# Kernel tuning notes

Measured on AMD Instinct MI355X. Metric: run time of the kernel, lower is better.

## Reference

```python
import jax, jax.numpy as jnp
import numpy as np

EMBED = 512
HEADS = 8                      # num_heads
HD = EMBED // HEADS // 2       # diff-attn head dim = 32
EXP = 4
DEPTH = 1
LAMBDA_INIT = 0.8 - 0.6 * float(np.exp(-0.3 * (DEPTH - 1)))  # 0.2
EPS = 1e-5


def layernorm(x, w, b):
    mu = jnp.mean(x, axis=-1, keepdims=True)
    var = jnp.mean(jnp.square(x - mu), axis=-1, keepdims=True)
    return (x - mu) * jax.lax.rsqrt(var + EPS) * w + b


def rmsnorm(x, w):
    ms = jnp.mean(jnp.square(x), axis=-1, keepdims=True)
    return x * jax.lax.rsqrt(ms + EPS) * w


def setup_inputs() -> dict:
    key = jax.random.key(0)
    ks = jax.random.split(key, 12)
    B, N, D = 8, 1024, EMBED
    s = 0.02
    inp = {
        "x": jax.random.normal(ks[0], (B, N, D), jnp.float32),
        # diff-attention params
        "Wq": jax.random.normal(ks[1], (D, D), jnp.float32) * s,
        "Wk": jax.random.normal(ks[2], (D, D), jnp.float32) * s,
        "Wv": jax.random.normal(ks[3], (D, D), jnp.float32) * s,
        "Wo": jax.random.normal(ks[4], (D, D), jnp.float32) * s,
        "lq1": jax.random.normal(ks[5], (HD,), jnp.float32) * 0.1,
        "lk1": jax.random.normal(ks[6], (HD,), jnp.float32) * 0.1,
        "lq2": jax.random.normal(ks[7], (HD,), jnp.float32) * 0.1,
        "lk2": jax.random.normal(ks[8], (HD,), jnp.float32) * 0.1,
        "subln_w": jnp.ones((2 * HD,), jnp.float32),
        # block norms
        "n1_w": jnp.ones((D,), jnp.float32), "n1_b": jnp.zeros((D,), jnp.float32),
        "n2_w": jnp.ones((D,), jnp.float32), "n2_b": jnp.zeros((D,), jnp.float32),
        # MLP: LN(D) -> Linear(D,4D) -> GELU -> LN(4D) -> Linear(4D,D)
        "mln1_w": jnp.ones((D,), jnp.float32), "mln1_b": jnp.zeros((D,), jnp.float32),
        "mW1": jax.random.normal(ks[9], (EXP * D, D), jnp.float32) * s,
        "mb1": jnp.zeros((EXP * D,), jnp.float32),
        "mln2_w": jnp.ones((EXP * D,), jnp.float32), "mln2_b": jnp.zeros((EXP * D,), jnp.float32),
        "mW2": jax.random.normal(ks[10], (D, EXP * D), jnp.float32) * s,
        "mb2": jnp.zeros((D,), jnp.float32),
    }
    return inp


def diff_attn(x, Wq, Wk, Wv, Wo, lq1, lk1, lq2, lk2, subln_w):
    B, N, D = x.shape
    q = (x @ Wq.T).reshape(B, N, 2 * HEADS, HD).transpose(0, 2, 1, 3)   # [B,2H,N,hd]
    k = (x @ Wk.T).reshape(B, N, 2 * HEADS, HD).transpose(0, 2, 1, 3)   # [B,2H,N,hd]
    v = (x @ Wv.T).reshape(B, N, HEADS, 2 * HD).transpose(0, 2, 1, 3)   # [B,H,N,2hd]
    q = q * (HD ** -0.5)
    scores = jnp.einsum("bhnd,bhmd->bhnm", q, k)                        # [B,2H,N,N]
    attn = jax.nn.softmax(scores, axis=-1)
    attn = attn.reshape(B, HEADS, 2, N, N)
    lam1 = jnp.exp(jnp.sum(lq1 * lk1))
    lam2 = jnp.exp(jnp.sum(lq2 * lk2))
    lam = lam1 - lam2 + LAMBDA_INIT
    attn = attn[:, :, 0] - lam * attn[:, :, 1]                          # [B,H,N,N]
    out = jnp.einsum("bhnm,bhmd->bhnd", attn, v)                        # [B,H,N,2hd]
    out = rmsnorm(out, subln_w) * (1.0 - LAMBDA_INIT)
    out = out.transpose(0, 2, 1, 3).reshape(B, N, D)
    return out @ Wo.T


def reference(x, Wq, Wk, Wv, Wo, lq1, lk1, lq2, lk2, subln_w,
              n1_w, n1_b, n2_w, n2_b,
              mln1_w, mln1_b, mW1, mb1, mln2_w, mln2_b, mW2, mb2):
    x_res = x
    xn = layernorm(x, n1_w, n1_b)
    a = diff_attn(xn, Wq, Wk, Wv, Wo, lq1, lk1, lq2, lk2, subln_w)
    h = layernorm(a, n2_w, n2_b) + x_res
    # MLP
    z = layernorm(h, mln1_w, mln1_b)
    z = jax.nn.gelu(z @ mW1.T + mb1, approximate=False)
    z = layernorm(z, mln2_w, mln2_b)
    z = z @ mW2.T + mb2
    return z + h
```

## Files before the change

### kernel.cpp

```cpp
#include <hip/hip_runtime.h>
#include <cstdint>
#include <cstddef>

typedef unsigned short u16;
typedef unsigned int   u32;
typedef __attribute__((ext_vector_type(8))) short short8;
typedef __attribute__((ext_vector_type(4))) float floatx4;

__device__ __forceinline__ float asf(u32 u){ union{u32 u; float f;} v; v.u=u; return v.f; }
__device__ __forceinline__ u32 asu(float f){ union{float f; u32 u;} v; v.f=f; return v.u; }
__device__ __forceinline__ u16 f2bf(float f){ u32 u = asu(f); u32 r = u + 0x7FFFu + ((u>>16)&1u); return (u16)(r>>16); }
__device__ __forceinline__ u16 f2bf_fast(float f){ return (u16)((asu(f) + 0x8000u)>>16); }
__device__ __forceinline__ u32 pack2(float a, float b){ return (u32)f2bf(a) | (((u32)f2bf(b))<<16); }
__device__ __forceinline__ void bf8f(uint4 d, float* o){
  o[0]=asf(d.x<<16); o[1]=asf(d.x&0xFFFF0000u);
  o[2]=asf(d.y<<16); o[3]=asf(d.y&0xFFFF0000u);
  o[4]=asf(d.z<<16); o[5]=asf(d.z&0xFFFF0000u);
  o[6]=asf(d.w<<16); o[7]=asf(d.w&0xFFFF0000u);
}

__global__ __launch_bounds__(256) void cvt_all(
    const float* __restrict__ Wq, const float* __restrict__ Wk,
    const float* __restrict__ Wv, const float* __restrict__ Wo,
    const float* __restrict__ W1, const float* __restrict__ W2,
    u16* __restrict__ Wqkv, u16* __restrict__ Wob,
    u16* __restrict__ W1b, u16* __restrict__ W2b)
{
  const int blk = blockIdx.x;
  const float* src; u16* dst; int off;
  if      (blk < 128)  { src = Wq; dst = Wqkv;          off = blk; }
  else if (blk < 256)  { src = Wk; dst = Wqkv + 262144; off = blk - 128; }
  else if (blk < 384)  { src = Wv; dst = Wqkv + 524288; off = blk - 256; }
  else if (blk < 512)  { src = Wo; dst = Wob;           off = blk - 384; }
  else if (blk < 1024) { src = W1; dst = W1b;           off = blk - 512; }
  else                 { src = W2; dst = W2b;           off = blk - 1024; }
  const int i = (off*256 + threadIdx.x)*8;
  const float4 a = *(const float4*)(src + i);
  const float4 b = *(const float4*)(src + i + 4);
  uint4 st;
  st.x = pack2(a.x, a.y); st.y = pack2(a.z, a.w);
  st.z = pack2(b.x, b.y); st.w = pack2(b.z, b.w);
  *(uint4*)(dst + i) = st;
}

enum { EPI_NONE=0, EPI_BIAS_GELU=1, EPI_BIAS_RES=2 };

template<int BM, int EPI, typename OutT>
__global__ __launch_bounds__(256) void gemm_bt(
    const u16* __restrict__ A, const u16* __restrict__ B,
    const float* __restrict__ bias, const float* __restrict__ res,
    OutT* __restrict__ C, int M, int N, int K)
{
  __shared__ u16 As[2][BM*32];
  __shared__ u16 Bs[2][128*32];
  const int tid  = threadIdx.x;
  const int wave = tid >> 6;
  const int lane = tid & 63;
  const int bm = blockIdx.y, bn = blockIdx.x;

  const int srow = wave*16 + (lane>>2);
  const int scol = (lane&3)*8;
  const u16* Ag = A + (size_t)bm*BM*K;
  const u16* Bg = B + (size_t)bn*128*K;

  constexpr int WM = BM/2;
  constexpr int MI = WM/16;
  const int wm = (wave>>1)*WM;
  const int wn = (wave&1)*64;
  const int fr = lane & 15;
  const int fk = (lane>>4)*8;

  floatx4 acc[MI][4] = {};

  #define G_STAGE(buf, kk)                                                        \
    do {                                                                          \
      if constexpr (BM == 128) {                                                  \
        _Pragma("unroll")                                                         \
        for (int tt = 0; tt < 2; ++tt)                                            \
          __builtin_amdgcn_global_load_lds(                                       \
              (__attribute__((address_space(1))) void*)(Ag + (tt*64 + srow)*K + (kk) + scol), \
              (__attribute__((address_space(3))) void*)(&As[buf][(tt*64 + wave*16)*32]),      \
              16, 0, 0);                                                          \
      } else {                                                                    \
        __builtin_amdgcn_global_load_lds(                                         \
            (__attribute__((address_space(1))) void*)(Ag + srow*K + (kk) + scol), \
            (__attribute__((address_space(3))) void*)(&As[buf][wave*16*32]),      \
            16, 0, 0);                                                            \
      }                                                                           \
      _Pragma("unroll")                                                           \
      for (int tt = 0; tt < 2; ++tt)                                              \
        __builtin_amdgcn_global_load_lds(                                         \
            (__attribute__((address_space(1))) void*)(Bg + (tt*64 + srow)*K + (kk) + scol), \
            (__attribute__((address_space(3))) void*)(&Bs[buf][(tt*64 + wave*16)*32]),      \
            16, 0, 0);                                                            \
    } while (0)

  G_STAGE(0, 0);
  __syncthreads();

  const int nsteps = K >> 5;
  for (int s = 0; s < nsteps; ++s) {
    const int cur = s & 1;
    if (s + 1 < nsteps) G_STAGE(cur^1, (s+1)*32);

    short8 af[MI], bfr[4];
    #pragma unroll
    for (int i=0;i<MI;i++) af[i] = *(const short8*)(&As[cur][(wm + i*16 + fr)*32 + fk]);
    #pragma unroll
    for (int j=0;j<4;j++) bfr[j] = *(const short8*)(&Bs[cur][(wn + j*16 + fr)*32 + fk]);
    #pragma unroll
    for (int i=0;i<MI;i++)
      #pragma unroll
      for (int j=0;j<4;j++)
        acc[i][j] = __builtin_amdgcn_mfma_f32_16x16x32_bf16(af[i], bfr[j], acc[i][j], 0, 0, 0);

    if (s + 1 < nsteps) __syncthreads();
  }
  #undef G_STAGE

  const int col0 = bn*128 + wn + fr;
  float bv[4] = {0.f,0.f,0.f,0.f};
  if constexpr (EPI != EPI_NONE) {
    #pragma unroll
    for (int j=0;j<4;j++) bv[j] = bias[col0 + j*16];
  }
  const int rq = (lane>>4)*4;
  #pragma unroll
  for (int i=0;i<MI;i++){
    #pragma unroll
    for (int rr=0;rr<4;rr++){
      const int m = bm*BM + wm + i*16 + rq + rr;
      const size_t rowoff = (size_t)m*N;
      #pragma unroll
      for (int j=0;j<4;j++){
        float vv = acc[i][j][rr];
        const int n = col0 + j*16;
        if constexpr (EPI == EPI_BIAS_GELU){
          vv += bv[j];
          vv = 0.5f*vv*(1.f + erff(vv*0.70710678118654752f));
        } else if constexpr (EPI == EPI_BIAS_RES){
          vv += bv[j] + res[rowoff + n];
        }
        if constexpr (sizeof(OutT) == 2) C[rowoff + n] = f2bf(vv);
        else                             C[rowoff + n] = vv;
      }
    }
  }
}

__global__ __launch_bounds__(256) void ln512_kernel(
    const float* __restrict__ x, const float* __restrict__ w, const float* __restrict__ b,
    u16* __restrict__ out)
{
  const int row  = blockIdx.x*4 + (threadIdx.x>>6);
  const int lane = threadIdx.x & 63;
  const size_t base = (size_t)row*512 + lane*8;
  float v[8];
  { const float4 a = *(const float4*)(x + base);
    const float4 c = *(const float4*)(x + base + 4);
    v[0]=a.x; v[1]=a.y; v[2]=a.z; v[3]=a.w; v[4]=c.x; v[5]=c.y; v[6]=c.z; v[7]=c.w; }
  float s=0.f, sq=0.f;
  #pragma unroll
  for (int i=0;i<8;i++){ s += v[i]; sq += v[i]*v[i]; }
  for (int off=32; off>0; off>>=1){ s += __shfl_xor(s, off, 64); sq += __shfl_xor(sq, off, 64); }
  const float mu = s*(1.f/512.f);
  const float rs = rsqrtf(sq*(1.f/512.f) - mu*mu + 1e-5f);
  float o[8];
  #pragma unroll
  for (int i=0;i<8;i++)
    o[i] = (v[i]-mu)*rs*w[lane*8+i] + b[lane*8+i];
  uint4 st; st.x=pack2(o[0],o[1]); st.y=pack2(o[2],o[3]); st.z=pack2(o[4],o[5]); st.w=pack2(o[6],o[7]);
  *(uint4*)(out + base) = st;
}

__global__ __launch_bounds__(256) void lnres_kernel(
    const u16* __restrict__ ao, const float* __restrict__ x,
    const float* __restrict__ w2, const float* __restrict__ b2,
    const float* __restrict__ w3, const float* __restrict__ b3,
    float* __restrict__ h, u16* __restrict__ z)
{
  const int row  = blockIdx.x*4 + (threadIdx.x>>6);
  const int lane = threadIdx.x & 63;
  const size_t base = (size_t)row*512 + lane*8;
  float a[8], xr[8];
  bf8f(*(const uint4*)(ao + base), a);
  { const float4 p = *(const float4*)(x + base);
    const float4 q = *(const float4*)(x + base + 4);
    xr[0]=p.x; xr[1]=p.y; xr[2]=p.z; xr[3]=p.w; xr[4]=q.x; xr[5]=q.y; xr[6]=q.z; xr[7]=q.w; }
  float s=0.f, sq=0.f;
  #pragma unroll
  for (int i=0;i<8;i++){ s += a[i]; sq += a[i]*a[i]; }
  for (int off=32; off>0; off>>=1){ s += __shfl_xor(s, off, 64); sq += __shfl_xor(sq, off, 64); }
  float mu = s*(1.f/512.f);
  float rs = rsqrtf(sq*(1.f/512.f) - mu*mu + 1e-5f);
  float hv[8];
  #pragma unroll
  for (int i=0;i<8;i++)
    hv[i] = (a[i]-mu)*rs*w2[lane*8+i] + b2[lane*8+i] + xr[i];
  { float4 p; p.x=hv[0]; p.y=hv[1]; p.z=hv[2]; p.w=hv[3];
    float4 q; q.x=hv[4]; q.y=hv[5]; q.z=hv[6]; q.w=hv[7];
    *(float4*)(h + base) = p; *(float4*)(h + base + 4) = q; }
  s=0.f; sq=0.f;
  #pragma unroll
  for (int i=0;i<8;i++){ s += hv[i]; sq += hv[i]*hv[i]; }
  for (int off=32; off>0; off>>=1){ s += __shfl_xor(s, off, 64); sq += __shfl_xor(sq, off, 64); }
  mu = s*(1.f/512.f);
  rs = rsqrtf(sq*(1.f/512.f) - mu*mu + 1e-5f);
  float zv[8];
  #pragma unroll
  for (int i=0;i<8;i++)
    zv[i] = (hv[i]-mu)*rs*w3[lane*8+i] + b3[lane*8+i];
  uint4 st; st.x=pack2(zv[0],zv[1]); st.y=pack2(zv[2],zv[3]); st.z=pack2(zv[4],zv[5]); st.w=pack2(zv[6],zv[7]);
  *(uint4*)(z + base) = st;
}

__global__ __launch_bounds__(256) void ln2048_kernel(
    const u16* x, const float* __restrict__ w, const float* __restrict__ b,
    u16* out)
{
  const int row  = blockIdx.x*4 + (threadIdx.x>>6);
  const int lane = threadIdx.x & 63;
  const u16* xp = x + (size_t)row*2048;
  float v[32];
  #pragma unroll
  for (int g=0; g<4; ++g) bf8f(*(const uint4*)(xp + g*512 + lane*8), v + g*8);
  float s=0.f, sq=0.f;
  #pragma unroll
  for (int i=0;i<32;i++){ s += v[i]; sq += v[i]*v[i]; }
  for (int off=32; off>0; off>>=1){ s += __shfl_xor(s, off, 64); sq += __shfl_xor(sq, off, 64); }
  const float mu = s*(1.f/2048.f);
  const float rs = rsqrtf(sq*(1.f/2048.f) - mu*mu + 1e-5f);
  u16* op = out + (size_t)row*2048;
  #pragma unroll
  for (int g=0; g<4; ++g){
    float o[8];
    #pragma unroll
    for (int i=0;i<8;i++){
      const int idx = g*512 + lane*8 + i;
      o[i] = (v[g*8+i]-mu)*rs*w[idx] + b[idx];
    }
    uint4 st; st.x=pack2(o[0],o[1]); st.y=pack2(o[2],o[3]); st.z=pack2(o[4],o[5]); st.w=pack2(o[6],o[7]);
    *(uint4*)(op + g*512 + lane*8) = st;
  }
}

__global__ __launch_bounds__(256) void transpose_v(
    const u16* __restrict__ QKV, u16* __restrict__ Vt)
{
  __shared__ __align__(16) u16 T[64][72];
  const int bid = blockIdx.x;
  const int bh  = bid >> 4;
  const int kt  = bid & 15;
  const int b   = bh >> 3;
  const int h   = bh & 7;
  const int tid = threadIdx.x;

  const int key = tid >> 2;
  const int dc  = (tid & 3) * 16;
  const u16* src = QKV + ((size_t)(b*1024 + kt*64 + key))*1536 + 1024 + h*64 + dc;
  const uint4 a0 = *(const uint4*)(src);
  const uint4 a1 = *(const uint4*)(src + 8);
  *(uint4*)(&T[key][dc])     = a0;
  *(uint4*)(&T[key][dc + 8]) = a1;
  __syncthreads();

  const int d  = tid >> 2;
  const int kc = (tid & 3) * 16;
  union { uint4 q[2]; u16 us[16]; } ow;
  #pragma unroll
  for (int i=0;i<16;i++) ow.us[i] = T[kc + i][d];
  u16* dst = Vt + ((size_t)(bh*64 + d))*1024 + kt*64 + kc;
  *(uint4*)(dst)     = ow.q[0];
  *(uint4*)(dst + 8) = ow.q[1];
}

#define ATT_SCALE 0.17677669529663687f

__global__ __launch_bounds__(256) void attn_mfma(
    const u16* __restrict__ QKV, const u16* __restrict__ Vt,
    const float* __restrict__ lq1, const float* __restrict__ lk1,
    const float* __restrict__ lq2, const float* __restrict__ lk2,
    const float* __restrict__ subw, u16* __restrict__ out)
{
  __shared__ __align__(16) u16 Ks1[2][64*32];
  __shared__ __align__(16) u16 Ks2[2][64*32];
  __shared__ __align__(16) u16 Vs [2][64*64];
  __shared__ __align__(16) u16 Ps [2][4][16*32];

  const int tid  = threadIdx.x;
  const int wave = tid >> 6;
  const int lane = tid & 63;
  const int quad = lane >> 4;
  const int l15  = lane & 15;

  const int bid = blockIdx.x;
  const int bh  = bid >> 4;
  const int qt  = bid & 15;
  const int b   = bh >> 3;
  const int h   = bh & 7;

  float t1 = 0.f, t2 = 0.f;
  for (int i=0;i<32;i++){ t1 += lq1[i]*lk1[i]; t2 += lq2[i]*lk2[i]; }
  const float lam = __expf(t1) - __expf(t2) + 0.2f;

  const int qrowg = b*1024 + qt*64 + wave*16 + l15;
  const short8 aq1 = *(const short8*)(QKV + (size_t)qrowg*1536 + 2*h*32 + quad*8);
  const short8 aq2 = *(const short8*)(QKV + (size_t)qrowg*1536 + 2*h*32 + 32 + quad*8);

  floatx4 O1[4] = {}, O2[4] = {};
  float l1acc[4] = {0.f,0.f,0.f,0.f};
  float l2acc[4] = {0.f,0.f,0.f,0.f};
  const floatx4 zf4 = {0.f,0.f,0.f,0.f};

  const int kvbase = b*1024;
  u16* pw1 = &Ps[0][wave][0];
  u16* pw2 = &Ps[1][wave][0];

  const int kchunk = ((lane&3) ^ ((lane>>3)&3)) * 8;
  const u16* KbaseS = QKV + (size_t)(kvbase + wave*16 + (lane>>2))*1536 + 512 + 2*h*32 + kchunk;
  const int vchunk = ((lane&7) ^ (lane>>3)) * 8;
  const u16* VbaseS = Vt + ((size_t)bh*64 + wave*16 + (lane>>3))*1024 + vchunk;

  #define STAGE_TILE(buf, tt)                                                     \
    do {                                                                          \
      const u16* kp = KbaseS + (size_t)(tt)*64*1536;                              \
      __builtin_amdgcn_global_load_lds(                                           \
          (__attribute__((address_space(1))) void*)(kp),                          \
          (__attribute__((address_space(3))) void*)(&Ks1[buf][wave*16*32]), 16, 0, 0); \
      __builtin_amdgcn_global_load_lds(                                           \
          (__attribute__((address_space(1))) void*)(kp + 32),                     \
          (__attribute__((address_space(3))) void*)(&Ks2[buf][wave*16*32]), 16, 0, 0); \
      const u16* vp = VbaseS + (tt)*64;                                           \
      __builtin_amdgcn_global_load_lds(                                           \
          (__attribute__((address_space(1))) void*)(vp),                          \
          (__attribute__((address_space(3))) void*)(&Vs[buf][wave*16*64]), 16, 0, 0); \
      __builtin_amdgcn_global_load_lds(                                           \
          (__attribute__((address_space(1))) void*)(vp + (size_t)8*1024),         \
          (__attribute__((address_space(3))) void*)(&Vs[buf][(wave*16+8)*64]), 16, 0, 0); \
    } while (0)

  STAGE_TILE(0, 0);
  __syncthreads();

  const int kslotR = (quad ^ ((l15>>1)&3)) * 8;
  const int pslotR = ((quad + (l15>>2)) & 3) * 8;

  for (int t = 0; t < 16; ++t) {
    const int cur = t & 1;

    if (t < 15) STAGE_TILE(cur^1, t+1);

    #pragma unroll
    for (int kh = 0; kh < 2; ++kh) {
      #pragma unroll
      for (int ktl = 0; ktl < 2; ++ktl) {
        const int kt = kh*2 + ktl;
        const short8 bk1 = *(const short8*)(&Ks1[cur][(kt*16 + l15)*32 + kslotR]);
        const short8 bk2 = *(const short8*)(&Ks2[cur][(kt*16 + l15)*32 + kslotR]);
        const floatx4 s1 = __builtin_amdgcn_mfma_f32_16x16x32_bf16(aq1, bk1, zf4, 0, 0, 0);
        const floatx4 s2 = __builtin_amdgcn_mfma_f32_16x16x32_bf16(aq2, bk2, zf4, 0, 0, 0);
        const int wslot = ((ktl*2 + (l15>>3) + quad) & 3)*8;
        u16* d1 = pw1 + wslot + (l15&7);
        u16* d2 = pw2 + wslot + (l15&7);
        #pragma unroll
        for (int rr = 0; rr < 4; ++rr) {
          const float p1 = __expf(s1[rr]*ATT_SCALE);
          const float p2 = __expf(s2[rr]*ATT_SCALE);
          d1[(quad*4+rr)*32] = f2bf_fast(p1);
          d2[(quad*4+rr)*32] = f2bf_fast(p2);
          l1acc[rr] += p1;
          l2acc[rr] += p2;
        }
      }
      const short8 ap1 = *(const short8*)(pw1 + l15*32 + pslotR);
      const short8 ap2 = *(const short8*)(pw2 + l15*32 + pslotR);
      const int vslotR = ((kh*4 + quad) ^ (l15&7)) * 8;
      #pragma unroll
      for (int nt = 0; nt < 4; ++nt) {
        const short8 bv = *(const short8*)(&Vs[cur][(nt*16 + l15)*64 + vslotR]);
        O1[nt] = __builtin_amdgcn_mfma_f32_16x16x32_bf16(ap1, bv, O1[nt], 0, 0, 0);
        O2[nt] = __builtin_amdgcn_mfma_f32_16x16x32_bf16(ap2, bv, O2[nt], 0, 0, 0);
      }
    }

    if (t < 15) __syncthreads();
  }
  #undef STAGE_TILE

  #pragma unroll
  for (int rr=0; rr<4; ++rr){
    float v1 = l1acc[rr], v2 = l2acc[rr];
    v1 += __shfl_xor(v1, 1, 64); v2 += __shfl_xor(v2, 1, 64);
    v1 += __shfl_xor(v1, 2, 64); v2 += __shfl_xor(v2, 2, 64);
    v1 += __shfl_xor(v1, 4, 64); v2 += __shfl_xor(v2, 4, 64);
    v1 += __shfl_xor(v1, 8, 64); v2 += __shfl_xor(v2, 8, 64);
    l1acc[rr] = v1; l2acc[rr] = v2;
  }

  float sw[4];
  #pragma unroll
  for (int nt=0; nt<4; ++nt) sw[nt] = subw[nt*16 + l15];

  #pragma unroll
  for (int rr=0; rr<4; ++rr){
    const int row = quad*4 + rr;
    const float il1 = 1.f / l1acc[rr];
    const float cl2 = lam / l2acc[rr];
    float o[4]; float ss = 0.f;
    #pragma unroll
    for (int nt=0; nt<4; ++nt){
      o[nt] = O1[nt][rr]*il1 - O2[nt][rr]*cl2;
      ss += o[nt]*o[nt];
    }
    ss += __shfl_xor(ss, 1, 64);
    ss += __shfl_xor(ss, 2, 64);
    ss += __shfl_xor(ss, 4, 64);
    ss += __shfl_xor(ss, 8, 64);
    const float rs = rsqrtf(ss*(1.f/64.f) + 1e-5f) * 0.8f;
    const int orow = b*1024 + qt*64 + wave*16 + row;
    u16* op = out + (size_t)orow*512 + h*64 + l15;
    #pragma unroll
    for (int nt=0; nt<4; ++nt)
      op[nt*16] = f2bf(o[nt]*rs*sw[nt]);
  }
}

extern "C" void kernel_launch(void* const* d_in, const int* in_sizes, int n_in,
                              void* d_out, int out_size, void* d_ws, size_t ws_size,
                              hipStream_t stream)
{
  (void)in_sizes; (void)n_in; (void)out_size; (void)ws_size;
  const float* x    = (const float*)d_in[0];
  const float* Wq   = (const float*)d_in[1];
  const float* Wk   = (const float*)d_in[2];
  const float* Wv   = (const float*)d_in[3];
  const float* Wo   = (const float*)d_in[4];
  const float* lq1  = (const float*)d_in[5];
  const float* lk1  = (const float*)d_in[6];
  const float* lq2  = (const float*)d_in[7];
  const float* lk2  = (const float*)d_in[8];
  const float* subw = (const float*)d_in[9];
  const float* n1w  = (const float*)d_in[10];
  const float* n1b  = (const float*)d_in[11];
  const float* n2w  = (const float*)d_in[12];
  const float* n2b  = (const float*)d_in[13];
  const float* m1w  = (const float*)d_in[14];
  const float* m1b  = (const float*)d_in[15];
  const float* mW1  = (const float*)d_in[16];
  const float* mb1  = (const float*)d_in[17];
  const float* m2w  = (const float*)d_in[18];
  const float* m2b  = (const float*)d_in[19];
  const float* mW2  = (const float*)d_in[20];
  const float* mb2  = (const float*)d_in[21];
  float* out = (float*)d_out;

  char* ws = (char*)d_ws;
  const size_t MB = (size_t)1 << 20;
  u16*  xn  = (u16*)(ws + 0*MB);
  u16*  qkv = (u16*)(ws + 8*MB);
  u16*  a   = (u16*)(ws + 0*MB);
  u16*  ao  = (u16*)(ws + 8*MB);
  u16*  z1  = (u16*)(ws + 16*MB);
  float* h  = (float*)(ws + 32*MB);
  u16*  vt  = (u16*)(ws + 32*MB);
  u16*  t   = (u16*)(ws + 48*MB);
  u16* Wqkvb= (u16*)(ws + 80*MB);
  u16* Wob  = (u16*)(ws + 81*MB + 512*1024);
  u16* W1b  = (u16*)(ws + 82*MB);
  u16* W2b  = (u16*)(ws + 84*MB);

  const int M = 8192;

  cvt_all<<<1536, 256, 0, stream>>>(Wq, Wk, Wv, Wo, mW1, mW2, Wqkvb, Wob, W1b, W2b);

  ln512_kernel<<<2048, 256, 0, stream>>>(x, n1w, n1b, xn);

  gemm_bt<64,EPI_NONE,u16><<<dim3(12,128), 256, 0, stream>>>(xn, Wqkvb, nullptr, nullptr, qkv, M, 1536, 512);

  transpose_v<<<1024, 256, 0, stream>>>(qkv, vt);

  attn_mfma<<<1024, 256, 0, stream>>>(qkv, vt, lq1, lk1, lq2, lk2, subw, a);

  gemm_bt<64,EPI_NONE,u16><<<dim3(4,128), 256, 0, stream>>>(a, Wob, nullptr, nullptr, ao, M, 512, 512);

  lnres_kernel<<<2048, 256, 0, stream>>>(ao, x, n2w, n2b, m1w, m1b, h, z1);

  gemm_bt<64,EPI_BIAS_GELU,u16><<<dim3(16,128), 256, 0, stream>>>(z1, W1b, mb1, nullptr, t, M, 2048, 512);

  ln2048_kernel<<<2048, 256, 0, stream>>>(t, m2w, m2b, t);

  gemm_bt<64,EPI_BIAS_RES,float><<<dim3(4,128), 256, 0, stream>>>(t, W2b, mb2, h, out, M, 512, 2048);
}
```

Baseline: 318.4 us.

## Deepen GEMM K-tile to 64 with XOR-swizzled LDS layout and remap attention blocks

The GEMM now stages 64-wide K slices instead of 32, which halves the number of barrier-synchronised steps and doubles the MFMA work done per sync. Each 16-byte chunk is placed in LDS at a column XOR-swizzled by its row, to avoid bank conflicts on the fragment reads. Shared memory per block doubles, which may reduce occupancy. The attention kernel's block-id mapping is also permuted, so neighbouring blocks handle different batch/head pairs and may spread load across XCDs or caches differently.

After: 305.2 us. -4.1%, faster.

```diff
diff --git a/kernel.cpp b/kernel.cpp
--- a/kernel.cpp
+++ b/kernel.cpp
@@ -51,15 +51,15 @@
     const float* __restrict__ bias, const float* __restrict__ res,
     OutT* __restrict__ C, int M, int N, int K)
 {
-  __shared__ u16 As[2][BM*32];
-  __shared__ u16 Bs[2][128*32];
+  __shared__ u16 As[2][BM*64];
+  __shared__ u16 Bs[2][128*64];
   const int tid  = threadIdx.x;
   const int wave = tid >> 6;
   const int lane = tid & 63;
   const int bm = blockIdx.y, bn = blockIdx.x;
 
-  const int srow = wave*16 + (lane>>2);
-  const int scol = (lane&3)*8;
+  const int srow8  = lane >> 3;
+  const int schunk = ((lane&7) ^ (lane>>3)) * 8;
   const u16* Ag = A + (size_t)bm*BM*K;
   const u16* Bg = B + (size_t)bn*128*K;
 
@@ -68,51 +68,55 @@
   const int wm = (wave>>1)*WM;
   const int wn = (wave&1)*64;
   const int fr = lane & 15;
-  const int fk = (lane>>4)*8;
+  const int quad = lane >> 4;
 
   floatx4 acc[MI][4] = {};
 
-  #define G_STAGE(buf, kk)                                                        \
+  #define G_STAGE(buf, koff)                                                      \
     do {                                                                          \
-      if constexpr (BM == 128) {                                                  \
-        _Pragma("unroll")                                                         \
-        for (int tt = 0; tt < 2; ++tt)                                            \
-          __builtin_amdgcn_global_load_lds(                                       \
-              (__attribute__((address_space(1))) void*)(Ag + (tt*64 + srow)*K + (kk) + scol), \
-              (__attribute__((address_space(3))) void*)(&As[buf][(tt*64 + wave*16)*32]),      \
-              16, 0, 0);                                                          \
-      } else {                                                                    \
+      _Pragma("unroll")                                                           \
+      for (int ii = 0; ii < BM/32; ++ii)                                          \
         __builtin_amdgcn_global_load_lds(                                         \
-            (__attribute__((address_space(1))) void*)(Ag + srow*K + (kk) + scol), \
-            (__attribute__((address_space(3))) void*)(&As[buf][wave*16*32]),      \
+            (__attribute__((address_space(1))) void*)(Ag + (size_t)(wave*(BM/4) + ii*8 + srow8)*K + (koff) + schunk), \
+            (__attribute__((address_space(3))) void*)(&As[buf][(wave*(BM/4) + ii*8)*64]), \
             16, 0, 0);                                                            \
-      }                                                                           \
       _Pragma("unroll")                                                           \
-      for (int tt = 0; tt < 2; ++tt)                                              \
+      for (int ii = 0; ii < 4; ++ii)                                              \
         __builtin_amdgcn_global_load_lds(                                         \
-            (__attribute__((address_space(1))) void*)(Bg + (tt*64 + srow)*K + (kk) + scol), \
-            (__attribute__((address_space(3))) void*)(&Bs[buf][(tt*64 + wave*16)*32]),      \
+            (__attribute__((address_space(1))) void*)(Bg + (size_t)(wave*32 + ii*8 + srow8)*K + (koff) + schunk), \
+            (__attribute__((address_space(3))) void*)(&Bs[buf][(wave*32 + ii*8)*64]), \
             16, 0, 0);                                                            \
     } while (0)
 
   G_STAGE(0, 0);
   __syncthreads();
 
-  const int nsteps = K >> 5;
+  const int nsteps = K >> 6;
   for (int s = 0; s < nsteps; ++s) {
     const int cur = s & 1;
-    if (s + 1 < nsteps) G_STAGE(cur^1, (s+1)*32);
-
-    short8 af[MI], bfr[4];
-    #pragma unroll
-    for (int i=0;i<MI;i++) af[i] = *(const short8*)(&As[cur][(wm + i*16 + fr)*32 + fk]);
-    #pragma unroll
-    for (int j=0;j<4;j++) bfr[j] = *(const short8*)(&Bs[cur][(wn + j*16 + fr)*32 + fk]);
-    #pragma unroll
-    for (int i=0;i<MI;i++)
-      #pragma unroll
-      for (int j=0;j<4;j++)
-        acc[i][j] = __builtin_amdgcn_mfma_f32_16x16x32_bf16(af[i], bfr[j], acc[i][j], 0, 0, 0);
+    if (s + 1 < nsteps) G_STAGE(cur^1, (s+1)*64);
+
+    short8 af[2][MI], bfr[2][4];
+    #pragma unroll
+    for (int kk=0; kk<2; ++kk){
+      #pragma unroll
+      for (int i=0;i<MI;i++){
+        const int row = wm + i*16 + fr;
+        af[kk][i] = *(const short8*)(&As[cur][row*64 + (((kk*4+quad) ^ (fr&7))*8)]);
+      }
+      #pragma unroll
+      for (int j=0;j<4;j++){
+        const int row = wn + j*16 + fr;
+        bfr[kk][j] = *(const short8*)(&Bs[cur][row*64 + (((kk*4+quad) ^ (fr&7))*8)]);
+      }
+    }
+    #pragma unroll
+    for (int kk=0; kk<2; ++kk)
+      #pragma unroll
+      for (int i=0;i<MI;i++)
+        #pragma unroll
+        for (int j=0;j<4;j++)
+          acc[i][j] = __builtin_amdgcn_mfma_f32_16x16x32_bf16(af[kk][i], bfr[kk][j], acc[i][j], 0, 0, 0);
 
     if (s + 1 < nsteps) __syncthreads();
   }
@@ -294,8 +298,8 @@
   const int l15  = lane & 15;
 
   const int bid = blockIdx.x;
-  const int bh  = bid >> 4;
-  const int qt  = bid & 15;
+  const int bh  = (bid & 7)*8 + ((bid >> 3) >> 4);
+  const int qt  = (bid >> 3) & 15;
   const int b   = bh >> 3;
   const int h   = bh & 7;
 
```

## Swizzle GEMM LDS layout, fold softmax scale into Q, remap attention blocks

Applied to the files above, without the earlier changes.

The GEMM tile staging now writes rows in an XOR-swizzled chunk order and reads them back with the matching swizzle, meant to remove LDS bank conflicts on the MFMA fragment loads. The QKV projection gains an epilogue that scales Q columns by scale*log2(e), so the attention kernel can use exp2f without a per-element multiply. The attention block index is remapped to interleave batch/head across consecutive blocks, which changes how work spreads over compute units and caches. The extra rounding from scaling Q before bf16 conversion slightly changes numerics.

New measurement: 323.4 us. Within noise of the previous version (+1.6%).

```diff
diff --git a/kernel.cpp b/kernel.cpp
--- a/kernel.cpp
+++ b/kernel.cpp
@@ -18,6 +18,8 @@
   o[4]=asf(d.z<<16); o[5]=asf(d.z&0xFFFF0000u);
   o[6]=asf(d.w<<16); o[7]=asf(d.w&0xFFFF0000u);
 }
+
+#define SC2 0.25503485966f
 
 __global__ __launch_bounds__(256) void cvt_all(
     const float* __restrict__ Wq, const float* __restrict__ Wk,
@@ -43,7 +45,7 @@
   *(uint4*)(dst + i) = st;
 }
 
-enum { EPI_NONE=0, EPI_BIAS_GELU=1, EPI_BIAS_RES=2 };
+enum { EPI_NONE=0, EPI_BIAS_GELU=1, EPI_BIAS_RES=2, EPI_QSCALE=3 };
 
 template<int BM, int EPI, typename OutT>
 __global__ __launch_bounds__(256) void gemm_bt(
@@ -58,8 +60,8 @@
   const int lane = tid & 63;
   const int bm = blockIdx.y, bn = blockIdx.x;
 
-  const int srow = wave*16 + (lane>>2);
-  const int scol = (lane&3)*8;
+  const int srow   = lane >> 2;
+  const int schunk = ((lane&3) ^ ((lane>>3)&3)) * 8;
   const u16* Ag = A + (size_t)bm*BM*K;
   const u16* Bg = B + (size_t)bn*128*K;
 
@@ -68,36 +70,30 @@
   const int wm = (wave>>1)*WM;
   const int wn = (wave&1)*64;
   const int fr = lane & 15;
-  const int fk = (lane>>4)*8;
+  const int quad = lane >> 4;
 
   floatx4 acc[MI][4] = {};
 
   #define G_STAGE(buf, kk)                                                        \
     do {                                                                          \
-      if constexpr (BM == 128) {                                                  \
-        _Pragma("unroll")                                                         \
-        for (int tt = 0; tt < 2; ++tt)                                            \
-          __builtin_amdgcn_global_load_lds(                                       \
-              (__attribute__((address_space(1))) void*)(Ag + (tt*64 + srow)*K + (kk) + scol), \
-              (__attribute__((address_space(3))) void*)(&As[buf][(tt*64 + wave*16)*32]),      \
-              16, 0, 0);                                                          \
-      } else {                                                                    \
+      _Pragma("unroll")                                                           \
+      for (int ii = 0; ii < BM/64; ++ii)                                          \
         __builtin_amdgcn_global_load_lds(                                         \
-            (__attribute__((address_space(1))) void*)(Ag + srow*K + (kk) + scol), \
-            (__attribute__((address_space(3))) void*)(&As[buf][wave*16*32]),      \
+            (__attribute__((address_space(1))) void*)(Ag + (size_t)(wave*(BM/4) + ii*16 + srow)*K + (kk) + schunk), \
+            (__attribute__((address_space(3))) void*)(&As[buf][(wave*(BM/4) + ii*16)*32]), \
             16, 0, 0);                                                            \
-      }                                                                           \
       _Pragma("unroll")                                                           \
-      for (int tt = 0; tt < 2; ++tt)                                              \
+      for (int ii = 0; ii < 2; ++ii)                                              \
         __builtin_amdgcn_global_load_lds(                                         \
-            (__attribute__((address_space(1))) void*)(Bg + (tt*64 + srow)*K + (kk) + scol), \
-            (__attribute__((address_space(3))) void*)(&Bs[buf][(tt*64 + wave*16)*32]),      \
+            (__attribute__((address_space(1))) void*)(Bg + (size_t)(wave*32 + ii*16 + srow)*K + (kk) + schunk), \
+            (__attribute__((address_space(3))) void*)(&Bs[buf][(wave*32 + ii*16)*32]), \
             16, 0, 0);                                                            \
     } while (0)
 
   G_STAGE(0, 0);
   __syncthreads();
 
+  const int aslot = (quad ^ ((fr>>1)&3)) * 8;
   const int nsteps = K >> 5;
   for (int s = 0; s < nsteps; ++s) {
     const int cur = s & 1;
@@ -105,9 +101,9 @@
 
     short8 af[MI], bfr[4];
     #pragma unroll
-    for (int i=0;i<MI;i++) af[i] = *(const short8*)(&As[cur][(wm + i*16 + fr)*32 + fk]);
-    #pragma unroll
-    for (int j=0;j<4;j++) bfr[j] = *(const short8*)(&Bs[cur][(wn + j*16 + fr)*32 + fk]);
+    for (int i=0;i<MI;i++) af[i]  = *(const short8*)(&As[cur][(wm + i*16 + fr)*32 + aslot]);
+    #pragma unroll
+    for (int j=0;j<4;j++)  bfr[j] = *(const short8*)(&Bs[cur][(wn + j*16 + fr)*32 + aslot]);
     #pragma unroll
     for (int i=0;i<MI;i++)
       #pragma unroll
@@ -120,7 +116,7 @@
 
   const int col0 = bn*128 + wn + fr;
   float bv[4] = {0.f,0.f,0.f,0.f};
-  if constexpr (EPI != EPI_NONE) {
+  if constexpr (EPI == EPI_BIAS_GELU || EPI == EPI_BIAS_RES) {
     #pragma unroll
     for (int j=0;j<4;j++) bv[j] = bias[col0 + j*16];
   }
@@ -140,6 +136,8 @@
           vv = 0.5f*vv*(1.f + erff(vv*0.70710678118654752f));
         } else if constexpr (EPI == EPI_BIAS_RES){
           vv += bv[j] + res[rowoff + n];
+        } else if constexpr (EPI == EPI_QSCALE){
+          if (n < 512) vv *= SC2;
         }
         if constexpr (sizeof(OutT) == 2) C[rowoff + n] = f2bf(vv);
         else                             C[rowoff + n] = vv;
@@ -274,8 +272,6 @@
   *(uint4*)(dst + 8) = ow.q[1];
 }
 
-#define ATT_SCALE 0.17677669529663687f
-
 __global__ __launch_bounds__(256) void attn_mfma(
     const u16* __restrict__ QKV, const u16* __restrict__ Vt,
     const float* __restrict__ lq1, const float* __restrict__ lk1,
@@ -294,8 +290,8 @@
   const int l15  = lane & 15;
 
   const int bid = blockIdx.x;
-  const int bh  = bid >> 4;
-  const int qt  = bid & 15;
+  const int bh  = (bid & 7)*8 + ((bid >> 3) >> 4);
+  const int qt  = (bid >> 3) & 15;
   const int b   = bh >> 3;
   const int h   = bh & 7;
 
@@ -364,8 +360,8 @@
         u16* d2 = pw2 + wslot + (l15&7);
         #pragma unroll
         for (int rr = 0; rr < 4; ++rr) {
-          const float p1 = __expf(s1[rr]*ATT_SCALE);
-          const float p2 = __expf(s2[rr]*ATT_SCALE);
+          const float p1 = exp2f(s1[rr]);
+          const float p2 = exp2f(s2[rr]);
           d1[(quad*4+rr)*32] = f2bf_fast(p1);
           d2[(quad*4+rr)*32] = f2bf_fast(p2);
           l1acc[rr] += p1;
@@ -475,7 +471,7 @@
 
   ln512_kernel<<<2048, 256, 0, stream>>>(x, n1w, n1b, xn);
 
-  gemm_bt<64,EPI_NONE,u16><<<dim3(12,128), 256, 0, stream>>>(xn, Wqkvb, nullptr, nullptr, qkv, M, 1536, 512);
+  gemm_bt<64,EPI_QSCALE,u16><<<dim3(12,128), 256, 0, stream>>>(xn, Wqkvb, nullptr, nullptr, qkv, M, 1536, 512);
 
   transpose_v<<<1024, 256, 0, stream>>>(qkv, vt);
 
```
